# Kernel tuning notes

Measured on AMD Instinct MI355X. Metric: run time of the kernel, lower is better.

Reference implementation:

```python
import jax, jax.numpy as jnp
import numpy as np

B, T, E, C, I = 4, 2048, 8, 1024, 2048

def setup_inputs() -> dict:
    key = jax.random.key(0)
    k1, k2, k3, k4 = jax.random.split(key, 4)
    x = jax.random.normal(k1, (B, T, C), dtype=jnp.float32)
    routing_weights = jax.random.uniform(k2, (B, T, E), dtype=jnp.float32)
    w1 = jax.random.normal(k3, (E, C, I), dtype=jnp.float32)
    w2 = jax.random.normal(k4, (E, I, C), dtype=jnp.float32)
    return {"x": x, "routing_weights": routing_weights, "w1": w1, "w2": w2}

def reference(x, routing_weights, w1, w2):
    # [B,T,C] x [E,C,I] -> [B,T,E,I]
    h = jnp.einsum('btc,eci->btei', x, w1)
    h = jax.nn.gelu(h, approximate=False)  # torch F.gelu default is exact erf
    # [B,T,E,I] x [E,I,C] -> [B,T,E,C]
    experts_out = jnp.einsum('btei,eic->btec', h, w2)
    # weighted combine over experts -> [B,T,C]
    agg = jnp.einsum('btec,bte->btc', experts_out, routing_weights)
    return (agg, experts_out)
```

## Files before the change

kernel.cpp:

```cpp
#include <hip/hip_runtime.h>
#include <hip/hip_bf16.h>


typedef unsigned short u16;
typedef __bf16 v8bf __attribute__((ext_vector_type(8)));
typedef float  v4f  __attribute__((ext_vector_type(4)));

#define M_TOT 8192
#define E_DIM 8
#define C_DIM 1024
#define I_DIM 2048

__device__ inline u16 f2b(float f) {
    __hip_bfloat16 h = __float2bfloat16(f);
    return *reinterpret_cast<u16*>(&h);
}

__device__ inline float fast_gelu(float x) {
    float x2 = x * x;
    float z  = x * fmaf(0.0356774081f, x2, 0.7978845608f);
    float u  = __expf(2.0f * z);
    float th = fmaf(-2.0f, __builtin_amdgcn_rcpf(u + 1.0f), 1.0f);
    return 0.5f * x * (1.0f + th);
}

__device__ inline void gload16(const u16* g, u16* l) {
    __builtin_amdgcn_global_load_lds(
        (const __attribute__((address_space(1))) void*)g,
        (__attribute__((address_space(3))) void*)l,
        16, 0, 0);
}


__global__ __launch_bounds__(256) void cvt_x_kernel(const float* __restrict__ x,
                                                    u16* __restrict__ xb) {
    int idx = blockIdx.x * 256 + threadIdx.x;
    float4 v = reinterpret_cast<const float4*>(x)[idx];
    ushort4 o;
    o.x = f2b(v.x); o.y = f2b(v.y); o.z = f2b(v.z); o.w = f2b(v.w);
    reinterpret_cast<ushort4*>(xb)[idx] = o;
}

__global__ __launch_bounds__(256) void transpose_cvt_kernel(const float* __restrict__ in,
                                                            u16* __restrict__ out,
                                                            int R, int Cd) {
    __shared__ float tile[32][33];
    int e = blockIdx.z;
    const float* ip = in + (size_t)e * R * Cd;
    u16* op = out + (size_t)e * R * Cd;
    int c0 = blockIdx.x * 32, r0 = blockIdx.y * 32;
    int tx = threadIdx.x & 31;
    int ty = threadIdx.x >> 5;
#pragma unroll
    for (int k = 0; k < 4; k++)
        tile[ty + 8 * k][tx] = ip[(size_t)(r0 + ty + 8 * k) * Cd + c0 + tx];
    __syncthreads();
#pragma unroll
    for (int k = 0; k < 4; k++)
        op[(size_t)(c0 + ty + 8 * k) * R + r0 + tx] = f2b(tile[tx][ty + 8 * k]);
}

template<int K>
__device__ inline void gemm_core(const u16* __restrict__ A, const u16* __restrict__ Bt,
                                 u16* ldsA, u16* ldsB, int m0, int n0, v4f (&acc)[8][4]) {
    constexpr int NS = K / 32;
    const int t = threadIdx.x, w = t >> 6, l = t & 63;
    const int wm = w >> 2, wn = w & 3;

    const u16* asrc[2]; const u16* bsrc[2]; int adst[2];
#pragma unroll
    for (int u = 0; u < 2; ++u) {
        int f = u * 8192 + w * 1024 + l * 16;
        int g = f ^ (((f >> 7) & 3) << 4);
        int row = g >> 6, col = (g >> 1) & 31;
        asrc[u] = A  + (size_t)(m0 + row) * K + col;
        bsrc[u] = Bt + (size_t)(n0 + row) * K + col;
        adst[u] = u * 4096 + w * 512;
    }

    const int lr = l & 15, lk = l >> 4;
    int aoffE[8], boffE[4];
#pragma unroll
    for (int i = 0; i < 8; ++i) {
        int g = (wm * 128 + i * 16 + lr) * 64 + lk * 16;
        aoffE[i] = (g ^ (((g >> 7) & 3) << 4)) >> 1;
    }
#pragma unroll
    for (int j = 0; j < 4; ++j) {
        int g = (wn * 64 + j * 16 + lr) * 64 + lk * 16;
        boffE[j] = (g ^ (((g >> 7) & 3) << 4)) >> 1;
    }

    auto STAGE = [&](int ks) {
        u16* la = ldsA + (ks & 3) * 8192;
        u16* lb = ldsB + (ks & 3) * 8192;
        int ko = ks * 32;
        gload16(asrc[0] + ko, la + adst[0]);
        gload16(asrc[1] + ko, la + adst[1]);
        gload16(bsrc[0] + ko, lb + adst[0]);
        gload16(bsrc[1] + ko, lb + adst[1]);
    };

#pragma unroll
    for (int i = 0; i < 8; ++i)
#pragma unroll
        for (int j = 0; j < 4; ++j) acc[i][j] = (v4f){0.f, 0.f, 0.f, 0.f};

    STAGE(0); STAGE(1); STAGE(2);
    asm volatile("s_waitcnt vmcnt(8)" ::: "memory");
    __builtin_amdgcn_s_barrier();

    for (int s = 0; s < NS; ++s) {
        const u16* as = ldsA + (s & 3) * 8192;
        const u16* bs = ldsB + (s & 3) * 8192;
        v8bf af[8], bfr[4];
#pragma unroll
        for (int i = 0; i < 8; ++i) af[i] = *(const v8bf*)(as + aoffE[i]);
#pragma unroll
        for (int j = 0; j < 4; ++j) bfr[j] = *(const v8bf*)(bs + boffE[j]);
        if (s < NS - 3) STAGE(s + 3);
        __builtin_amdgcn_s_setprio(1);
#pragma unroll
        for (int i = 0; i < 8; ++i)
#pragma unroll
            for (int j = 0; j < 4; ++j)
                acc[i][j] = __builtin_amdgcn_mfma_f32_16x16x32_bf16(af[i], bfr[j], acc[i][j], 0, 0, 0);
        __builtin_amdgcn_s_setprio(0);
        if (s < NS - 3)       asm volatile("s_waitcnt vmcnt(8)" ::: "memory");
        else if (s == NS - 3) asm volatile("s_waitcnt vmcnt(4)" ::: "memory");
        else if (s == NS - 2) asm volatile("s_waitcnt vmcnt(0)" ::: "memory");
        if (s < NS - 1) __builtin_amdgcn_s_barrier();
    }
}

__global__ __launch_bounds__(512, 2) void gemm1_kernel(const u16* __restrict__ A,
                                                       const u16* __restrict__ w1T,
                                                       u16* __restrict__ H,
                                                       int e_base, size_t h_stride) {
    __shared__ __align__(16) u16 lds[65536];
    int e = e_base + blockIdx.z;
    const u16* Bt = w1T + (size_t)e * I_DIM * C_DIM;
    u16* Hp = H + (size_t)blockIdx.z * h_stride;
    int m0 = blockIdx.y * 256, n0 = blockIdx.x * 256;

    v4f acc[8][4];
    gemm_core<C_DIM>(A, Bt, lds, lds + 32768, m0, n0, acc);

    int l = threadIdx.x & 63, w = threadIdx.x >> 6;
    int wm = w >> 2, wn = w & 3;
    int lr4 = (l >> 4) * 4, lc = l & 15;
#pragma unroll
    for (int i = 0; i < 8; ++i) {
        int mg = m0 + wm * 128 + i * 16 + lr4;
#pragma unroll
        for (int j = 0; j < 4; ++j) {
            int ng = n0 + wn * 64 + j * 16 + lc;
#pragma unroll
            for (int r = 0; r < 4; ++r)
                Hp[(size_t)(mg + r) * I_DIM + ng] = f2b(fast_gelu(acc[i][j][r]));
        }
    }
}

__global__ __launch_bounds__(512, 2) void gemm2_kernel(const u16* __restrict__ H,
                                                       const u16* __restrict__ w2T,
                                                       float* __restrict__ EO,
                                                       int e_base, size_t h_stride) {
    __shared__ __align__(16) u16 lds[65536];
    int e = e_base + blockIdx.z;
    const u16* A  = H + (size_t)blockIdx.z * h_stride;
    const u16* Bt = w2T + (size_t)e * C_DIM * I_DIM;
    int m0 = blockIdx.y * 256, n0 = blockIdx.x * 256;

    v4f acc[8][4];
    gemm_core<I_DIM>(A, Bt, lds, lds + 32768, m0, n0, acc);

    int l = threadIdx.x & 63, w = threadIdx.x >> 6;
    int wm = w >> 2, wn = w & 3;
    int lr4 = (l >> 4) * 4, lc = l & 15;
#pragma unroll
    for (int i = 0; i < 8; ++i) {
        int mg = m0 + wm * 128 + i * 16 + lr4;
#pragma unroll
        for (int j = 0; j < 4; ++j) {
            int ng = n0 + wn * 64 + j * 16 + lc;
#pragma unroll
            for (int r = 0; r < 4; ++r)
                EO[((size_t)(mg + r) * E_DIM + e) * C_DIM + ng] = acc[i][j][r];
        }
    }
}

__global__ __launch_bounds__(256) void combine_kernel(const float* __restrict__ EO,
                                                      const float* __restrict__ Rw,
                                                      float* __restrict__ agg) {
    int idx = blockIdx.x * 256 + threadIdx.x;
    int m = idx >> 8, cq = idx & 255;
    const float4* eo4 = reinterpret_cast<const float4*>(EO);
    float4 s = make_float4(0.f, 0.f, 0.f, 0.f);
#pragma unroll
    for (int e = 0; e < E_DIM; e++) {
        float r = Rw[m * E_DIM + e];
        float4 v = eo4[((size_t)m * E_DIM + e) * 256 + cq];
        s.x += r * v.x; s.y += r * v.y; s.z += r * v.z; s.w += r * v.w;
    }
    reinterpret_cast<float4*>(agg)[(size_t)m * 256 + cq] = s;
}

extern "C" void kernel_launch(void* const* d_in, const int* in_sizes, int n_in,
                              void* d_out, int out_size, void* d_ws, size_t ws_size,
                              hipStream_t stream) {
    const float* x  = (const float*)d_in[0];
    const float* rw = (const float*)d_in[1];
    const float* w1 = (const float*)d_in[2];
    const float* w2 = (const float*)d_in[3];

    float* agg = (float*)d_out;
    float* EO  = agg + (size_t)M_TOT * C_DIM;

    u16* xb  = (u16*)d_ws;
    u16* w1T = xb  + (size_t)M_TOT * C_DIM;
    u16* w2T = w1T + (size_t)E_DIM * I_DIM * C_DIM;
    u16* h   = w2T + (size_t)E_DIM * C_DIM * I_DIM;

    size_t elems_before_h = (size_t)M_TOT * C_DIM + 2 * (size_t)E_DIM * I_DIM * C_DIM;
    size_t h_per_expert   = (size_t)M_TOT * I_DIM;
    bool batched = ws_size >= (elems_before_h + (size_t)E_DIM * h_per_expert) * sizeof(u16);

    cvt_x_kernel<<<(M_TOT * C_DIM) / 1024, 256, 0, stream>>>(x, xb);
    transpose_cvt_kernel<<<dim3(I_DIM / 32, C_DIM / 32, E_DIM), 256, 0, stream>>>(w1, w1T, C_DIM, I_DIM);
    transpose_cvt_kernel<<<dim3(C_DIM / 32, I_DIM / 32, E_DIM), 256, 0, stream>>>(w2, w2T, I_DIM, C_DIM);

    if (batched) {
        gemm1_kernel<<<dim3(I_DIM / 256, M_TOT / 256, E_DIM), 512, 0, stream>>>(
            xb, w1T, h, 0, h_per_expert);
        gemm2_kernel<<<dim3(C_DIM / 256, M_TOT / 256, E_DIM), 512, 0, stream>>>(
            h, w2T, EO, 0, h_per_expert);
    } else {
        for (int e = 0; e < E_DIM; e++) {
            gemm1_kernel<<<dim3(I_DIM / 256, M_TOT / 256, 1), 512, 0, stream>>>(
                xb, w1T, h, e, 0);
            gemm2_kernel<<<dim3(C_DIM / 256, M_TOT / 256, 1), 512, 0, stream>>>(
                h, w2T, EO, e, 0);
        }
    }

    combine_kernel<<<M_TOT, 256, 0, stream>>>(EO, rw, agg);
}
```

Measured before the change: 1.049 ms.

## Split K-step into two MFMA phases with interleaved loads and remap block grid

Each K-step of the GEMM core is split into two halves. The A-tile global prefetch is issued before the first 4x4 MFMA block and the B-tile prefetch before the second, with extra barriers and LDS waits between them, so memory traffic is interleaved with compute in a ping-pong style. The launch grid also becomes 1D with the expert index in the low bits, so consecutive blocks work on different experts, which changes L2 reuse and how work is spread across CUs. The cost is extra barriers per K-step and a possible loss of reuse of shared input tiles between neighbouring blocks.

```diff
diff --git a/kernel.cpp b/kernel.cpp
--- a/kernel.cpp
+++ b/kernel.cpp
@@ -91,12 +91,15 @@
         boffE[j] = (g ^ (((g >> 7) & 3) << 4)) >> 1;
     }
 
-    auto STAGE = [&](int ks) {
+    auto STAGE_A = [&](int ks) {
         u16* la = ldsA + (ks & 3) * 8192;
-        u16* lb = ldsB + (ks & 3) * 8192;
         int ko = ks * 32;
         gload16(asrc[0] + ko, la + adst[0]);
         gload16(asrc[1] + ko, la + adst[1]);
+    };
+    auto STAGE_B = [&](int ks) {
+        u16* lb = ldsB + (ks & 3) * 8192;
+        int ko = ks * 32;
         gload16(bsrc[0] + ko, lb + adst[0]);
         gload16(bsrc[1] + ko, lb + adst[1]);
     };
@@ -106,7 +109,7 @@
 #pragma unroll
         for (int j = 0; j < 4; ++j) acc[i][j] = (v4f){0.f, 0.f, 0.f, 0.f};
 
-    STAGE(0); STAGE(1); STAGE(2);
+    STAGE_A(0); STAGE_B(0); STAGE_A(1); STAGE_B(1); STAGE_A(2); STAGE_B(2);
     asm volatile("s_waitcnt vmcnt(8)" ::: "memory");
     __builtin_amdgcn_s_barrier();
 
@@ -115,13 +118,28 @@
         const u16* bs = ldsB + (s & 3) * 8192;
         v8bf af[8], bfr[4];
 #pragma unroll
-        for (int i = 0; i < 8; ++i) af[i] = *(const v8bf*)(as + aoffE[i]);
+        for (int i = 0; i < 4; ++i) af[i] = *(const v8bf*)(as + aoffE[i]);
 #pragma unroll
         for (int j = 0; j < 4; ++j) bfr[j] = *(const v8bf*)(bs + boffE[j]);
-        if (s < NS - 3) STAGE(s + 3);
+        if (s < NS - 3) STAGE_A(s + 3);
+        __builtin_amdgcn_s_barrier();
+        asm volatile("s_waitcnt lgkmcnt(0)" ::: "memory");
         __builtin_amdgcn_s_setprio(1);
 #pragma unroll
-        for (int i = 0; i < 8; ++i)
+        for (int i = 0; i < 4; ++i)
+#pragma unroll
+            for (int j = 0; j < 4; ++j)
+                acc[i][j] = __builtin_amdgcn_mfma_f32_16x16x32_bf16(af[i], bfr[j], acc[i][j], 0, 0, 0);
+        __builtin_amdgcn_s_setprio(0);
+        __builtin_amdgcn_s_barrier();
+#pragma unroll
+        for (int i = 4; i < 8; ++i) af[i] = *(const v8bf*)(as + aoffE[i]);
+        if (s < NS - 3) STAGE_B(s + 3);
+        __builtin_amdgcn_s_barrier();
+        asm volatile("s_waitcnt lgkmcnt(0)" ::: "memory");
+        __builtin_amdgcn_s_setprio(1);
+#pragma unroll
+        for (int i = 4; i < 8; ++i)
 #pragma unroll
             for (int j = 0; j < 4; ++j)
                 acc[i][j] = __builtin_amdgcn_mfma_f32_16x16x32_bf16(af[i], bfr[j], acc[i][j], 0, 0, 0);
@@ -136,12 +154,16 @@
 __global__ __launch_bounds__(512, 2) void gemm1_kernel(const u16* __restrict__ A,
                                                        const u16* __restrict__ w1T,
                                                        u16* __restrict__ H,
-                                                       int e_base, size_t h_stride) {
+                                                       int e_base, int nE, size_t h_stride) {
     __shared__ __align__(16) u16 lds[65536];
-    int e = e_base + blockIdx.z;
+    int id = blockIdx.x;
+    int e, j;
+    if (nE == E_DIM) { e = id & 7; j = id >> 3; }
+    else             { e = e_base; j = id; }
+    int n0 = (j & 7) * 256;
+    int m0 = (j >> 3) * 256;
     const u16* Bt = w1T + (size_t)e * I_DIM * C_DIM;
-    u16* Hp = H + (size_t)blockIdx.z * h_stride;
-    int m0 = blockIdx.y * 256, n0 = blockIdx.x * 256;
+    u16* Hp = H + (size_t)(e - e_base) * h_stride;
 
     v4f acc[8][4];
     gemm_core<C_DIM>(A, Bt, lds, lds + 32768, m0, n0, acc);
@@ -153,11 +175,11 @@
     for (int i = 0; i < 8; ++i) {
         int mg = m0 + wm * 128 + i * 16 + lr4;
 #pragma unroll
-        for (int j = 0; j < 4; ++j) {
-            int ng = n0 + wn * 64 + j * 16 + lc;
+        for (int j2 = 0; j2 < 4; ++j2) {
+            int ng = n0 + wn * 64 + j2 * 16 + lc;
 #pragma unroll
             for (int r = 0; r < 4; ++r)
-                Hp[(size_t)(mg + r) * I_DIM + ng] = f2b(fast_gelu(acc[i][j][r]));
+                Hp[(size_t)(mg + r) * I_DIM + ng] = f2b(fast_gelu(acc[i][j2][r]));
         }
     }
 }
@@ -165,12 +187,16 @@
 __global__ __launch_bounds__(512, 2) void gemm2_kernel(const u16* __restrict__ H,
                                                        const u16* __restrict__ w2T,
                                                        float* __restrict__ EO,
-                                                       int e_base, size_t h_stride) {
+                                                       int e_base, int nE, size_t h_stride) {
     __shared__ __align__(16) u16 lds[65536];
-    int e = e_base + blockIdx.z;
-    const u16* A  = H + (size_t)blockIdx.z * h_stride;
+    int id = blockIdx.x;
+    int e, j;
+    if (nE == E_DIM) { e = id & 7; j = id >> 3; }
+    else             { e = e_base; j = id; }
+    int n0 = (j & 3) * 256;
+    int m0 = (j >> 2) * 256;
+    const u16* A  = H + (size_t)(e - e_base) * h_stride;
     const u16* Bt = w2T + (size_t)e * C_DIM * I_DIM;
-    int m0 = blockIdx.y * 256, n0 = blockIdx.x * 256;
 
     v4f acc[8][4];
     gemm_core<I_DIM>(A, Bt, lds, lds + 32768, m0, n0, acc);
@@ -182,11 +208,11 @@
     for (int i = 0; i < 8; ++i) {
         int mg = m0 + wm * 128 + i * 16 + lr4;
 #pragma unroll
-        for (int j = 0; j < 4; ++j) {
-            int ng = n0 + wn * 64 + j * 16 + lc;
+        for (int j2 = 0; j2 < 4; ++j2) {
+            int ng = n0 + wn * 64 + j2 * 16 + lc;
 #pragma unroll
             for (int r = 0; r < 4; ++r)
-                EO[((size_t)(mg + r) * E_DIM + e) * C_DIM + ng] = acc[i][j][r];
+                EO[((size_t)(mg + r) * E_DIM + e) * C_DIM + ng] = acc[i][j2][r];
         }
     }
 }
@@ -232,16 +258,12 @@
     transpose_cvt_kernel<<<dim3(C_DIM / 32, I_DIM / 32, E_DIM), 256, 0, stream>>>(w2, w2T, I_DIM, C_DIM);
 
     if (batched) {
-        gemm1_kernel<<<dim3(I_DIM / 256, M_TOT / 256, E_DIM), 512, 0, stream>>>(
-            xb, w1T, h, 0, h_per_expert);
-        gemm2_kernel<<<dim3(C_DIM / 256, M_TOT / 256, E_DIM), 512, 0, stream>>>(
-            h, w2T, EO, 0, h_per_expert);
+        gemm1_kernel<<<E_DIM * 8 * 32, 512, 0, stream>>>(xb, w1T, h, 0, E_DIM, h_per_expert);
+        gemm2_kernel<<<E_DIM * 4 * 32, 512, 0, stream>>>(h, w2T, EO, 0, E_DIM, h_per_expert);
     } else {
         for (int e = 0; e < E_DIM; e++) {
-            gemm1_kernel<<<dim3(I_DIM / 256, M_TOT / 256, 1), 512, 0, stream>>>(
-                xb, w1T, h, e, 0);
-            gemm2_kernel<<<dim3(C_DIM / 256, M_TOT / 256, 1), 512, 0, stream>>>(
-                h, w2T, EO, e, 0);
+            gemm1_kernel<<<8 * 32, 512, 0, stream>>>(xb, w1T, h, e, 1, 0);
+            gemm2_kernel<<<4 * 32, 512, 0, stream>>>(h, w2T, EO, e, 1, 0);
         }
     }
 
```

Measured after the change: 1.005 ms. 4.1% less time.
